# Kernel tuning notes

Hardware: AMD Instinct MI355X
Metric: run time of the kernel (lower is better)

The kernel has to match this reference:

```python
import jax, jax.numpy as jnp
import numpy as np

N_HEADS, INPUT_DIM, EMBED_DIM = 8, 128, 128
KEY_DIM = EMBED_DIM // N_HEADS  # val_dim = key_dim = 16
B, N = 8, 1024


def setup_inputs() -> dict:
    key = jax.random.key(0)
    ks = jax.random.split(key, 16)
    stdv_k = 1.0 / np.sqrt(KEY_DIM)
    stdv_e = 1.0 / np.sqrt(EMBED_DIM)

    def U(k, shape, s):
        return jax.random.uniform(k, shape, jnp.float32, -s, s)

    hdk = (N_HEADS, INPUT_DIM, KEY_DIM)
    hke = (N_HEADS, KEY_DIM, EMBED_DIM)
    return {
        "q_n": jax.random.normal(ks[0], (B, N, INPUT_DIM), jnp.float32),
        "q_c": jax.random.normal(ks[1], (B, N, INPUT_DIM), jnp.float32),
        "mask": jax.random.bernoulli(ks[2], 0.5, (B, N, N)),
        "W_query_n": U(ks[3], hdk, stdv_k),
        "W_key_nn": U(ks[4], hdk, stdv_k),
        "W_val_nn": U(ks[5], hdk, stdv_k),
        "W_key_c": U(ks[6], hdk, stdv_k),
        "W_val_c": U(ks[7], hdk, stdv_k),
        "W_query_c": U(ks[8], hdk, stdv_k),
        "W_key_n": U(ks[9], hdk, stdv_k),
        "W_val_n": U(ks[10], hdk, stdv_k),
        "W_out_node": U(ks[11], hke, stdv_e),
        "W_out_color": U(ks[12], hke, stdv_e),
    }


def reference(q_n, q_c, mask, W_query_n, W_key_nn, W_val_nn, W_key_c, W_val_c,
              W_query_c, W_key_n, W_val_n, W_out_node, W_out_color):
    norm = 1.0 / jnp.sqrt(jnp.asarray(KEY_DIM, q_n.dtype))
    neg_inf = jnp.asarray(-jnp.inf, q_n.dtype)

    def proj(x, W):  # (B,N,D), (H,D,K) -> (H,B,N,K)
        return jnp.einsum('bnd,hdk->hbnk', x, W)

    # --- color stream: q_c attends over nodes q_n ---
    Q_c = proj(q_c, W_query_c)
    K_n = proj(q_n, W_key_n)
    V_n = proj(q_n, W_val_n)
    attn_c = jax.nn.softmax(norm * jnp.einsum('hbqk,hbnk->hbqn', Q_c, K_n), axis=-1)
    heads_c = jnp.einsum('hbqn,hbnv->hbqv', attn_c, V_n)
    out_color = jnp.einsum('hbqv,hve->bqe', heads_c, W_out_color)

    # --- node stream: masked self-attention + attention over colors ---
    Q_n = proj(q_n, W_query_n)
    K_nn = proj(q_n, W_key_nn)
    V_nn = proj(q_n, W_val_nn)
    comp_nn = norm * jnp.einsum('hbqk,hbnk->hbqn', Q_n, K_nn)
    m = mask[None]  # (1,B,Q,N) broadcast over heads; True = not allowed
    comp_nn = jnp.where(m, neg_inf, comp_nn)
    attn_nn = jax.nn.softmax(comp_nn, axis=-1)
    attn_nn = jnp.where(m, jnp.asarray(0.0, q_n.dtype), attn_nn)
    heads_nn = jnp.einsum('hbqn,hbnv->hbqv', attn_nn, V_nn)

    K_nc = proj(q_c, W_key_c)
    V_nc = proj(q_c, W_val_c)
    attn_nc = jax.nn.softmax(norm * jnp.einsum('hbqk,hbnk->hbqn', Q_n, K_nc), axis=-1)
    heads_nc = jnp.einsum('hbqn,hbnv->hbqv', attn_nc, V_nc)

    heads = heads_nn + heads_nc
    out = jnp.einsum('hbqv,hve->bqe', heads, W_out_node)
    return (out, out_color)
```

## Files before the change

kernel.cpp:

```cpp
#include <hip/hip_runtime.h>
#include <stdint.h>

#define NH 8
#define NB 8
#define NN 1024
#define ND 128
#define NK 16
#define NF (NB*NN)
#define C2EXP 0.36067376022224085f
#define LSTR 136

typedef float f32x16 __attribute__((ext_vector_type(16)));
typedef short bf16x8 __attribute__((ext_vector_type(8)));

__device__ __forceinline__ uint16_t f2bf(float f){
  uint32_t x = __float_as_uint(f);
  uint32_t r = (x + 0x7fffu + ((x>>16)&1u)) >> 16;
  return (uint16_t)r;
}
__device__ __forceinline__ float fast_exp2(float x){
#if __has_builtin(__builtin_amdgcn_exp2f)
  return __builtin_amdgcn_exp2f(x);
#else
  return exp2f(x);
#endif
}

__global__ __launch_bounds__(256) void pack_kernel(const int* __restrict__ mask,
                                                   uint32_t* __restrict__ packN,
                                                   uint16_t* __restrict__ onesw){
  if (blockIdx.x == 0) {
    for (int i = threadIdx.x; i < 1024; i += 256) onesw[i] = 0x3F80;
  }
  const int w = threadIdx.x >> 6, lane = threadIdx.x & 63;
  const int row = blockIdx.x*4 + w;
  const int* mp = mask + (size_t)row*NN;
  uint32_t* dst = packN + (size_t)row*32;
  for (int wq = 0; wq < 16; ++wq) {
    int v = mp[wq*64 + lane];
    unsigned long long bal = __ballot(v != 0);
    if (lane == 0) { dst[wq*2] = (uint32_t)bal; dst[wq*2+1] = (uint32_t)(bal>>32); }
  }
}

struct ProjArgs { const float* x[8]; const float* w[8]; };

__global__ __launch_bounds__(256) void proj_kernel(ProjArgs args, uint16_t* ws){
  __shared__ __align__(16) uint16_t WT[128*LSTR];
  __shared__ __align__(16) uint16_t S[128*LSTR];
  const int p = blockIdx.y;
  const int rb = blockIdx.x;
  const int tid = threadIdx.x;

  const float4* w4 = (const float4*)args.w[p];
  #pragma unroll
  for (int i = 0; i < 16; ++i) {
    int e4 = i*256 + tid;
    float4 f = w4[e4];
    int e = e4*4;
    int h = e >> 11, d = (e >> 4) & 127, k = e & 15;
    uint16_t* wr = &WT[(h*16 + k)*LSTR + d];
    wr[0*LSTR] = f2bf(f.x); wr[1*LSTR] = f2bf(f.y);
    wr[2*LSTR] = f2bf(f.z); wr[3*LSTR] = f2bf(f.w);
  }
  __syncthreads();

  const int wave = tid >> 6, lane = tid & 63;
  const int l5 = lane >> 5, lm = lane & 31;
  const int r0 = rb*128 + wave*32;
  const float* xrow = args.x[p] + (size_t)(r0 + lm)*ND + l5*8;

  bf16x8 afr[8];
  #pragma unroll
  for (int kt = 0; kt < 8; ++kt) {
    float4 f0 = *(const float4*)(xrow + kt*16);
    float4 f1 = *(const float4*)(xrow + kt*16 + 4);
    bf16x8 a;
    a[0]=f2bf(f0.x); a[1]=f2bf(f0.y); a[2]=f2bf(f0.z); a[3]=f2bf(f0.w);
    a[4]=f2bf(f1.x); a[5]=f2bf(f1.y); a[6]=f2bf(f1.z); a[7]=f2bf(f1.w);
    afr[kt] = a;
  }

  const bool tr = (p==2)|(p==5)|(p==7);
  const float qsc = (p==0 || p==3) ? C2EXP : 1.0f;
  #pragma unroll
  for (int nt = 0; nt < 4; ++nt) {
    f32x16 acc;
    #pragma unroll
    for (int i = 0; i < 16; ++i) acc[i] = 0.f;
    #pragma unroll
    for (int kt = 0; kt < 8; ++kt) {
      bf16x8 b = *(const bf16x8*)(&WT[(nt*32 + lm)*LSTR + kt*16 + l5*8]);
      acc = __builtin_amdgcn_mfma_f32_32x32x16_bf16(afr[kt], b, acc, 0, 0, 0);
    }
    #pragma unroll
    for (int i = 0; i < 16; ++i) {
      int r = wave*32 + (i&3) + 8*(i>>2) + 4*l5;
      int c = nt*32 + lm;
      if (tr) {
        int t2 = (r>>2)&3;
        int rp = (t2==1 || t2==2) ? (r^12) : r;
        S[c*LSTR + rp] = f2bf(acc[i]);
      } else {
        S[r*LSTR + c] = f2bf(acc[i]*qsc);
      }
    }
  }
  __syncthreads();

  uint16_t* dst = ws + (size_t)p*((size_t)NH*NF*NK);
  if (!tr) {
    #pragma unroll
    for (int it = 0; it < 8; ++it) {
      int c = it*256 + tid;
      int row = c >> 4, cg = c & 15;
      bf16x8 v = *(const bf16x8*)(&S[row*LSTR + cg*8]);
      int h = cg >> 1, k8 = cg & 1;
      *(bf16x8*)(dst + ((size_t)h*NF + rb*128 + row)*NK + k8*8) = v;
    }
  } else {
    const int b = rb >> 3, nb = (rb & 7)*128;
    #pragma unroll
    for (int it = 0; it < 8; ++it) {
      int c = it*256 + tid;
      int col = c >> 4, ng = c & 15;
      bf16x8 v = *(const bf16x8*)(&S[col*LSTR + ng*8]);
      int h = col >> 4, k = col & 15;
      *(bf16x8*)(dst + ((size_t)(h*NB + b)*NK + k)*NN + nb + ng*8) = v;
    }
  }
}

template<bool MASKED>
__device__ __forceinline__ void attn_stream(
    const uint4* __restrict__ kbuf, bf16x8 aq,
    const uint16_t* __restrict__ vbase, const uint4* __restrict__ pmw4,
    int nh, int l5, int lm, f32x16& O)
{
  f32x16 Z;
  #pragma unroll
  for (int i = 0; i < 16; ++i) Z[i] = 0.f;

  uint32_t mw[16];
  if (MASKED) {
    uint4 m0 = pmw4[nh*4+0], m1 = pmw4[nh*4+1];
    uint4 m2 = pmw4[nh*4+2], m3 = pmw4[nh*4+3];
    mw[0]=m0.x; mw[1]=m0.y; mw[2]=m0.z; mw[3]=m0.w;
    mw[4]=m1.x; mw[5]=m1.y; mw[6]=m1.z; mw[7]=m1.w;
    mw[8]=m2.x; mw[9]=m2.y; mw[10]=m2.z; mw[11]=m2.w;
    mw[12]=m3.x; mw[13]=m3.y; mw[14]=m3.z; mw[15]=m3.w;
  }

  const int base_n = nh*512;
  const bool vload = (lm < 17);

  bf16x8 av1, av2, av1n, av2n;
  #pragma unroll
  for (int i = 0; i < 8; ++i) { av1[i]=0; av2[i]=0; av1n[i]=0; av2n[i]=0; }
  if (vload) {
    const uint16_t* vp = vbase + base_n + l5*8;
    av1 = *(const bf16x8*)(vp);
    av2 = *(const bf16x8*)(vp + 16);
  }
  f32x16 Stc = __builtin_amdgcn_mfma_f32_32x32x16_bf16(
      *(const bf16x8*)(&kbuf[l5*1024 + base_n + lm]), aq, Z, 0, 0, 0);

  #pragma unroll
  for (int t = 0; t < 16; ++t) {
    f32x16 Stn;
    if (t < 15) {
      const int n1 = base_n + (t+1)*32;
      if (vload) {
        const uint16_t* vp = vbase + n1 + l5*8;
        av1n = *(const bf16x8*)(vp);
        av2n = *(const bf16x8*)(vp + 16);
      }
      Stn = __builtin_amdgcn_mfma_f32_32x32x16_bf16(
          *(const bf16x8*)(&kbuf[l5*1024 + n1 + lm]), aq, Z, 0, 0, 0);
    }

    const uint32_t mws = MASKED ? (mw[t] >> (4*l5)) : 0u;
    float p[16];
    #pragma unroll
    for (int i = 0; i < 16; ++i) {
      float pv = fast_exp2(Stc[i]);
      if (MASKED && ((mws >> ((i&3) + 8*(i>>2))) & 1u)) pv = 0.f;
      p[i] = pv;
    }
    union { uint32_t u[4]; bf16x8 v; } B1, B2;
    #pragma unroll
    for (int k = 0; k < 4; ++k) {
      B1.u[k] = __builtin_amdgcn_perm(__float_as_uint(p[2*k+1]),
                                      __float_as_uint(p[2*k]),   0x07060302u);
      B2.u[k] = __builtin_amdgcn_perm(__float_as_uint(p[2*k+9]),
                                      __float_as_uint(p[2*k+8]), 0x07060302u);
    }
    O = __builtin_amdgcn_mfma_f32_32x32x16_bf16(av1, B1.v, O, 0, 0, 0);
    O = __builtin_amdgcn_mfma_f32_32x32x16_bf16(av2, B2.v, O, 0, 0, 0);

    if (t < 15) { Stc = Stn; av1 = av1n; av2 = av2n; }
  }
}

__global__ __launch_bounds__(512, 4) void attn_kernel(
    const uint16_t* __restrict__ Qn_, const uint16_t* __restrict__ Qc_,
    const uint16_t* __restrict__ Knn, const uint16_t* __restrict__ VTnn,
    const uint16_t* __restrict__ Knc, const uint16_t* __restrict__ VTnc,
    const uint16_t* __restrict__ Knc_c, const uint16_t* __restrict__ VTc,
    const uint32_t* __restrict__ packN, const uint16_t* __restrict__ onesb,
    uint16_t* __restrict__ h_nn, uint16_t* __restrict__ h_nc,
    uint16_t* __restrict__ h_c)
{
  __shared__ uint4 kbuf[2048];
  const int z = blockIdx.z;
  const bool masked = (z == 0);
  const uint16_t* Q  = (z == 2) ? Qc_ : Qn_;
  const uint16_t* K  = (z == 0) ? Knn : (z == 1) ? Knc : Knc_c;
  const uint16_t* VT = (z == 0) ? VTnn : (z == 1) ? VTnc : VTc;
  uint16_t* outp     = (z == 0) ? h_nn : (z == 1) ? h_nc : h_c;

  const int hb = blockIdx.y;
  const int h = hb >> 3, b = hb & 7;
  const size_t base = ((size_t)h*NF + (size_t)b*NN)*NK;
  const int tid = threadIdx.x;

  const uint4* kg = (const uint4*)(K + base);
  for (int i = tid; i < 2048; i += 512)
    kbuf[(i & 1)*1024 + (i >> 1)] = kg[i];
  __syncthreads();

  const int wave = tid >> 6, lane = tid & 63;
  const int l5 = lane >> 5, lm = lane & 31;
  const int qt = wave & 3, nh = wave >> 2;
  const int q = blockIdx.x*128 + qt*32 + lm;

  const bf16x8 aq = *(const bf16x8*)(Q + base + (size_t)q*NK + l5*8);
  const uint4* pmw4 = (const uint4*)(packN + ((size_t)b*NN + q)*32);

  const uint16_t* VTb = VT + (size_t)hb*(NK*NN);
  const uint16_t* vb = (lm < 16) ? (VTb + (size_t)lm*NN) : onesb;

  f32x16 O;
  #pragma unroll
  for (int i = 0; i < 16; ++i) O[i] = 0.f;

  if (masked) attn_stream<true >(kbuf, aq, vb, pmw4, nh, l5, lm, O);
  else        attn_stream<false>(kbuf, aq, vb, nullptr, nh, l5, lm, O);

  float L = O[8] + __shfl_xor(O[8], 32, 64);

  __syncthreads();
  float* cw = ((float*)kbuf) + ((size_t)(qt*2 + l5)*32 + lm)*10;
  if (nh == 1) {
    #pragma unroll
    for (int i = 0; i < 8; ++i) cw[i] = O[i];
    cw[8] = L;
  }
  __syncthreads();
  if (nh == 0) {
    const float l = L + cw[8];
    const float il = (l > 0.f) ? 1.f/l : 0.f;
    uint32_t w[4];
    #pragma unroll
    for (int k = 0; k < 4; ++k) {
      float va = (O[2*k]   + cw[2*k])  *il;
      float vb2 = (O[2*k+1] + cw[2*k+1])*il;
      w[k] = ((uint32_t)f2bf(vb2) << 16) | f2bf(va);
    }
    uint16_t* hp = outp + ((size_t)b*NN + q)*128 + h*16 + l5*4;
    *(uint2*)(hp)     = make_uint2(w[0], w[1]);
    *(uint2*)(hp + 8) = make_uint2(w[2], w[3]);
  }
}

__global__ __launch_bounds__(256) void outproj_kernel(
    const uint16_t* __restrict__ hnn, const uint16_t* __restrict__ hnc,
    const uint16_t* __restrict__ hc,
    const float* __restrict__ wn, const float* __restrict__ wc,
    float* __restrict__ out)
{
  __shared__ __align__(16) uint16_t WT[128*LSTR];
  const int s = blockIdx.y;
  const int rb = blockIdx.x;
  const int tid = threadIdx.x;
  const float* wsrc = s ? wc : wn;
  const float4* w4 = (const float4*)wsrc;
  #pragma unroll
  for (int i = 0; i < 16; ++i) {
    int e4 = i*256 + tid;
    float4 f = w4[e4];
    int e = e4*4;
    int c = e >> 7, col = e & 127;
    uint16_t* wr = &WT[col*LSTR + c];
    wr[0*LSTR] = f2bf(f.x); wr[1*LSTR] = f2bf(f.y);
    wr[2*LSTR] = f2bf(f.z); wr[3*LSTR] = f2bf(f.w);
  }
  __syncthreads();

  const int wave = tid >> 6, lane = tid & 63;
  const int l5 = lane >> 5, lm = lane & 31;
  const int rt = wave & 1, nh2 = wave >> 1;
  const int r0 = rb*64 + rt*32;
  const size_t hoff = (size_t)(r0 + lm)*128 + l5*8;
  const uint16_t* hp1 = (s ? hc : hnn) + hoff;
  const uint16_t* hp2 = hnc + hoff;
  bf16x8 afr1[8], afr2[8];
  #pragma unroll
  for (int kt = 0; kt < 8; ++kt) {
    afr1[kt] = *(const bf16x8*)(hp1 + kt*16);
    if (!s) afr2[kt] = *(const bf16x8*)(hp2 + kt*16);
  }

  float* dst = out + (size_t)s*((size_t)NF*ND) + (size_t)r0*ND;
  #pragma unroll
  for (int nt2 = 0; nt2 < 2; ++nt2) {
    const int nt = nh2*2 + nt2;
    f32x16 acc;
    #pragma unroll
    for (int i = 0; i < 16; ++i) acc[i] = 0.f;
    #pragma unroll
    for (int kt = 0; kt < 8; ++kt) {
      bf16x8 b = *(const bf16x8*)(&WT[(nt*32 + lm)*LSTR + kt*16 + l5*8]);
      acc = __builtin_amdgcn_mfma_f32_32x32x16_bf16(afr1[kt], b, acc, 0, 0, 0);
      if (!s)
        acc = __builtin_amdgcn_mfma_f32_32x32x16_bf16(afr2[kt], b, acc, 0, 0, 0);
    }
    #pragma unroll
    for (int i = 0; i < 16; ++i) {
      int r = (i&3) + 8*(i>>2) + 4*l5;
      dst[(size_t)r*ND + nt*32 + lm] = acc[i];
    }
  }
}

extern "C" void kernel_launch(void* const* d_in, const int* in_sizes, int n_in,
                              void* d_out, int out_size, void* d_ws, size_t ws_size,
                              hipStream_t stream)
{
  const float* q_n = (const float*)d_in[0];
  const float* q_c = (const float*)d_in[1];
  const int* mask = (const int*)d_in[2];
  const float* W[10];
  for (int i = 0; i < 10; ++i) W[i] = (const float*)d_in[3+i];

  uint16_t* ws16 = (uint16_t*)d_ws;
  const size_t PE = (size_t)NH*NF*NK;
  uint16_t* Qc   = ws16 + 0*PE;
  uint16_t* Kn   = ws16 + 1*PE;
  uint16_t* VTn  = ws16 + 2*PE;
  uint16_t* Qn   = ws16 + 3*PE;
  uint16_t* Knn  = ws16 + 4*PE;
  uint16_t* VTnn = ws16 + 5*PE;
  uint16_t* Knc  = ws16 + 6*PE;
  uint16_t* VTnc = ws16 + 7*PE;
  uint16_t* heads_nn = ws16 + 8*PE;
  uint32_t* packN   = (uint32_t*)(ws16 + 9*PE);
  uint16_t* heads_c  = ws16 + 10*PE;
  uint16_t* heads_nc = ws16 + 11*PE;
  uint16_t* onesb    = ws16 + 12*PE;

  pack_kernel<<<2048, 256, 0, stream>>>(mask, packN, onesb);

  ProjArgs pa;
  pa.x[0]=q_c; pa.w[0]=W[5];
  pa.x[1]=q_n; pa.w[1]=W[6];
  pa.x[2]=q_n; pa.w[2]=W[7];
  pa.x[3]=q_n; pa.w[3]=W[0];
  pa.x[4]=q_n; pa.w[4]=W[1];
  pa.x[5]=q_n; pa.w[5]=W[2];
  pa.x[6]=q_c; pa.w[6]=W[3];
  pa.x[7]=q_c; pa.w[7]=W[4];
  proj_kernel<<<dim3(64, 8), 256, 0, stream>>>(pa, ws16);

  attn_kernel<<<dim3(8, 64, 3), 512, 0, stream>>>(
      Qn, Qc, Knn, VTnn, Knc, VTnc, Kn, VTn, packN, onesb,
      heads_nn, heads_nc, heads_c);

  outproj_kernel<<<dim3(128, 2), 256, 0, stream>>>(heads_nn, heads_nc, heads_c,
                                                   W[8], W[9], (float*)d_out);
}
```

Measured before the change: 167.4 us.

## Drop LDS key staging and split-N waves; each wave streams all keys

```diff
diff --git a/kernel.cpp b/kernel.cpp
--- a/kernel.cpp
+++ b/kernel.cpp
@@ -131,60 +131,78 @@
   }
 }
 
-template<bool MASKED>
-__device__ __forceinline__ void attn_stream(
-    const uint4* __restrict__ kbuf, bf16x8 aq,
-    const uint16_t* __restrict__ vbase, const uint4* __restrict__ pmw4,
-    int nh, int l5, int lm, f32x16& O)
+__global__ __launch_bounds__(256, 4) void attn_kernel(
+    const uint16_t* __restrict__ Qn_, const uint16_t* __restrict__ Qc_,
+    const uint16_t* __restrict__ Knn, const uint16_t* __restrict__ VTnn,
+    const uint16_t* __restrict__ Knc, const uint16_t* __restrict__ VTnc,
+    const uint16_t* __restrict__ Kc,  const uint16_t* __restrict__ VTc,
+    const uint32_t* __restrict__ packN, const uint16_t* __restrict__ onesb,
+    uint16_t* __restrict__ h_nn, uint16_t* __restrict__ h_nc,
+    uint16_t* __restrict__ h_c)
 {
+  const int z = blockIdx.z;
+  const bool masked = (z == 0);
+  const uint16_t* Q  = (z == 2) ? Qc_ : Qn_;
+  const uint16_t* K  = (z == 0) ? Knn : (z == 1) ? Knc : Kc;
+  const uint16_t* VT = (z == 0) ? VTnn : (z == 1) ? VTnc : VTc;
+  uint16_t* outp     = (z == 0) ? h_nn : (z == 1) ? h_nc : h_c;
+
+  const int hb = blockIdx.y;
+  const int h = hb >> 3, b = hb & 7;
+  const size_t base = ((size_t)h*NF + (size_t)b*NN)*NK;
+
+  const int wave = threadIdx.x >> 6, lane = threadIdx.x & 63;
+  const int l5 = lane >> 5, lm = lane & 31;
+  const int q = blockIdx.x*128 + wave*32 + lm;
+
+  const bf16x8 aq = *(const bf16x8*)(Q + base + (size_t)q*NK + l5*8);
+  const uint16_t* Kb = K + base;
+  const uint16_t* VTb = VT + (size_t)hb*(NK*NN);
+  const uint16_t* vb = (lm < 16) ? (VTb + (size_t)lm*NN) : onesb;
+  const bool vload = (lm < 17);
+  const uint32_t* packrow = packN + ((size_t)b*NN + q)*32;
+
   f32x16 Z;
-  #pragma unroll
-  for (int i = 0; i < 16; ++i) Z[i] = 0.f;
-
-  uint32_t mw[16];
-  if (MASKED) {
-    uint4 m0 = pmw4[nh*4+0], m1 = pmw4[nh*4+1];
-    uint4 m2 = pmw4[nh*4+2], m3 = pmw4[nh*4+3];
-    mw[0]=m0.x; mw[1]=m0.y; mw[2]=m0.z; mw[3]=m0.w;
-    mw[4]=m1.x; mw[5]=m1.y; mw[6]=m1.z; mw[7]=m1.w;
-    mw[8]=m2.x; mw[9]=m2.y; mw[10]=m2.z; mw[11]=m2.w;
-    mw[12]=m3.x; mw[13]=m3.y; mw[14]=m3.z; mw[15]=m3.w;
-  }
-
-  const int base_n = nh*512;
-  const bool vload = (lm < 17);
+  f32x16 O;
+  #pragma unroll
+  for (int i = 0; i < 16; ++i) { Z[i] = 0.f; O[i] = 0.f; }
 
   bf16x8 av1, av2, av1n, av2n;
   #pragma unroll
   for (int i = 0; i < 8; ++i) { av1[i]=0; av2[i]=0; av1n[i]=0; av2n[i]=0; }
   if (vload) {
-    const uint16_t* vp = vbase + base_n + l5*8;
-    av1 = *(const bf16x8*)(vp);
-    av2 = *(const bf16x8*)(vp + 16);
-  }
-  f32x16 Stc = __builtin_amdgcn_mfma_f32_32x32x16_bf16(
-      *(const bf16x8*)(&kbuf[l5*1024 + base_n + lm]), aq, Z, 0, 0, 0);
-
-  #pragma unroll
-  for (int t = 0; t < 16; ++t) {
+    av1 = *(const bf16x8*)(vb + l5*8);
+    av2 = *(const bf16x8*)(vb + l5*8 + 16);
+  }
+  uint32_t mwc = masked ? packrow[0] : 0u;
+  bf16x8 bk0 = *(const bf16x8*)(Kb + (size_t)lm*NK + l5*8);
+  bf16x8 bkc = *(const bf16x8*)(Kb + (size_t)(32 + lm)*NK + l5*8);
+  f32x16 Stc = __builtin_amdgcn_mfma_f32_32x32x16_bf16(bk0, aq, Z, 0, 0, 0);
+
+  #pragma unroll 4
+  for (int t = 0; t < 32; ++t) {
     f32x16 Stn;
-    if (t < 15) {
-      const int n1 = base_n + (t+1)*32;
+    bf16x8 bkn = bkc;
+    uint32_t mwn = 0;
+    if (t < 31) {
+      const int n1 = (t+1)*32;
       if (vload) {
-        const uint16_t* vp = vbase + n1 + l5*8;
+        const uint16_t* vp = vb + n1 + l5*8;
         av1n = *(const bf16x8*)(vp);
         av2n = *(const bf16x8*)(vp + 16);
       }
-      Stn = __builtin_amdgcn_mfma_f32_32x32x16_bf16(
-          *(const bf16x8*)(&kbuf[l5*1024 + n1 + lm]), aq, Z, 0, 0, 0);
-    }
-
-    const uint32_t mws = MASKED ? (mw[t] >> (4*l5)) : 0u;
+      if (t < 30)
+        bkn = *(const bf16x8*)(Kb + (size_t)((t+2)*32 + lm)*NK + l5*8);
+      Stn = __builtin_amdgcn_mfma_f32_32x32x16_bf16(bkc, aq, Z, 0, 0, 0);
+      if (masked) mwn = packrow[t+1];
+    }
+
+    const uint32_t mws = masked ? (mwc >> (4*l5)) : 0u;
     float p[16];
     #pragma unroll
     for (int i = 0; i < 16; ++i) {
       float pv = fast_exp2(Stc[i]);
-      if (MASKED && ((mws >> ((i&3) + 8*(i>>2))) & 1u)) pv = 0.f;
+      if (masked && ((mws >> ((i&3) + 8*(i>>2))) & 1u)) pv = 0.f;
       p[i] = pv;
     }
     union { uint32_t u[4]; bf16x8 v; } B1, B2;
@@ -198,79 +216,22 @@
     O = __builtin_amdgcn_mfma_f32_32x32x16_bf16(av1, B1.v, O, 0, 0, 0);
     O = __builtin_amdgcn_mfma_f32_32x32x16_bf16(av2, B2.v, O, 0, 0, 0);
 
-    if (t < 15) { Stc = Stn; av1 = av1n; av2 = av2n; }
-  }
-}
-
-__global__ __launch_bounds__(512, 4) void attn_kernel(
-    const uint16_t* __restrict__ Qn_, const uint16_t* __restrict__ Qc_,
-    const uint16_t* __restrict__ Knn, const uint16_t* __restrict__ VTnn,
-    const uint16_t* __restrict__ Knc, const uint16_t* __restrict__ VTnc,
-    const uint16_t* __restrict__ Knc_c, const uint16_t* __restrict__ VTc,
-    const uint32_t* __restrict__ packN, const uint16_t* __restrict__ onesb,
-    uint16_t* __restrict__ h_nn, uint16_t* __restrict__ h_nc,
-    uint16_t* __restrict__ h_c)
-{
-  __shared__ uint4 kbuf[2048];
-  const int z = blockIdx.z;
-  const bool masked = (z == 0);
-  const uint16_t* Q  = (z == 2) ? Qc_ : Qn_;
-  const uint16_t* K  = (z == 0) ? Knn : (z == 1) ? Knc : Knc_c;
-  const uint16_t* VT = (z == 0) ? VTnn : (z == 1) ? VTnc : VTc;
-  uint16_t* outp     = (z == 0) ? h_nn : (z == 1) ? h_nc : h_c;
-
-  const int hb = blockIdx.y;
-  const int h = hb >> 3, b = hb & 7;
-  const size_t base = ((size_t)h*NF + (size_t)b*NN)*NK;
-  const int tid = threadIdx.x;
-
-  const uint4* kg = (const uint4*)(K + base);
-  for (int i = tid; i < 2048; i += 512)
-    kbuf[(i & 1)*1024 + (i >> 1)] = kg[i];
-  __syncthreads();
-
-  const int wave = tid >> 6, lane = tid & 63;
-  const int l5 = lane >> 5, lm = lane & 31;
-  const int qt = wave & 3, nh = wave >> 2;
-  const int q = blockIdx.x*128 + qt*32 + lm;
-
-  const bf16x8 aq = *(const bf16x8*)(Q + base + (size_t)q*NK + l5*8);
-  const uint4* pmw4 = (const uint4*)(packN + ((size_t)b*NN + q)*32);
-
-  const uint16_t* VTb = VT + (size_t)hb*(NK*NN);
-  const uint16_t* vb = (lm < 16) ? (VTb + (size_t)lm*NN) : onesb;
-
-  f32x16 O;
-  #pragma unroll
-  for (int i = 0; i < 16; ++i) O[i] = 0.f;
-
-  if (masked) attn_stream<true >(kbuf, aq, vb, pmw4, nh, l5, lm, O);
-  else        attn_stream<false>(kbuf, aq, vb, nullptr, nh, l5, lm, O);
-
-  float L = O[8] + __shfl_xor(O[8], 32, 64);
-
-  __syncthreads();
-  float* cw = ((float*)kbuf) + ((size_t)(qt*2 + l5)*32 + lm)*10;
-  if (nh == 1) {
-    #pragma unroll
-    for (int i = 0; i < 8; ++i) cw[i] = O[i];
-    cw[8] = L;
-  }
-  __syncthreads();
-  if (nh == 0) {
-    const float l = L + cw[8];
-    const float il = (l > 0.f) ? 1.f/l : 0.f;
-    uint32_t w[4];
-    #pragma unroll
-    for (int k = 0; k < 4; ++k) {
-      float va = (O[2*k]   + cw[2*k])  *il;
-      float vb2 = (O[2*k+1] + cw[2*k+1])*il;
-      w[k] = ((uint32_t)f2bf(vb2) << 16) | f2bf(va);
-    }
-    uint16_t* hp = outp + ((size_t)b*NN + q)*128 + h*16 + l5*4;
-    *(uint2*)(hp)     = make_uint2(w[0], w[1]);
-    *(uint2*)(hp + 8) = make_uint2(w[2], w[3]);
-  }
+    if (t < 31) { Stc = Stn; av1 = av1n; av2 = av2n; bkc = bkn; mwc = mwn; }
+  }
+
+  const float L = O[8] + __shfl_xor(O[8], 32, 64);
+  const float il = (L > 0.f) ? 1.f/L : 0.f;
+
+  uint32_t w[4];
+  #pragma unroll
+  for (int k = 0; k < 4; ++k) {
+    float va = O[2*k]   * il;
+    float vb2 = O[2*k+1] * il;
+    w[k] = ((uint32_t)f2bf(vb2) << 16) | f2bf(va);
+  }
+  uint16_t* hp = outp + ((size_t)b*NN + q)*128 + h*16 + l5*4;
+  *(uint2*)(hp)     = make_uint2(w[0], w[1]);
+  *(uint2*)(hp + 8) = make_uint2(w[2], w[3]);
 }
 
 __global__ __launch_bounds__(256) void outproj_kernel(
@@ -372,7 +333,7 @@
   pa.x[7]=q_c; pa.w[7]=W[4];
   proj_kernel<<<dim3(64, 8), 256, 0, stream>>>(pa, ws16);
 
-  attn_kernel<<<dim3(8, 64, 3), 512, 0, stream>>>(
+  attn_kernel<<<dim3(8, 64, 3), 256, 0, stream>>>(
       Qn, Qc, Knn, VTnn, Knc, VTnc, Kn, VTn, packN, onesb,
       heads_nn, heads_nc, heads_c);
 
```

Result: slower. 180.4 us (+7.8%).
